# Kernel tuning notes

Hardware: AMD Instinct MI355X
Metric: run time of the kernel (lower is better)

## Reference

```python
import jax, jax.numpy as jnp
import numpy as np

B, T, V, F = 64, 2, 512, 512  # V == F required by the original loop indexing

def setup_inputs() -> dict:
    key = jax.random.key(0)
    x = jax.random.normal(key, (B, T, V, F), dtype=jnp.float32)
    return {"x": x}

def reference(x):
    # split along time axis into two halves; only the first slice of the first half is used
    xh, _ = jnp.split(x, 2, axis=1)
    x0 = xh[:, 0]  # (B, V, F)
    # Faithful to tf.norm(x[:, 0, i, :], ord=2) with NO axis: Frobenius norm over
    # the whole (batch, feature) slice -> one scalar per vertex.
    n = jnp.sqrt(jnp.sum(x0 * x0, axis=(0, 2)))  # (V,)
    # S[b,i,j] = sum_f x0[b,i,f] * x0[b,j,f]  (inner loop over j covers all V since V==F)
    gram = jnp.einsum('bif,bjf->bij', x0, x0)  # (B, V, V)
    return gram / (n[:, None] * n[None, :])
```

## Files before the change

kernel.cpp:

```cpp
#include <hip/hip_runtime.h>
#include <hip/hip_bf16.h>
#include <math.h>


#define BATCH 64
#define VDIM 512
#define FDIM 512
#define XBS (2 * VDIM * FDIM)
#define OBS (VDIM * VDIM)

typedef __bf16 bf16x8 __attribute__((ext_vector_type(8)));
typedef __bf16 bf16x4 __attribute__((ext_vector_type(4)));
typedef float f32x4 __attribute__((ext_vector_type(4)));

#define BM 128
#define BK 64
#define NKT (FDIM / BK)

#define INVN_OFF 33554432

#define GLL16(g, l)                                                          \
    __builtin_amdgcn_global_load_lds(                                        \
        (const __attribute__((address_space(1))) void*)(g),                  \
        (__attribute__((address_space(3))) void*)(l), 16, 0, 0)

__global__ __launch_bounds__(512) void cvt_norm_kernel(const float* __restrict__ x,
                                                       __bf16* __restrict__ xb,
                                                       float* __restrict__ inv_n) {
    const int v = blockIdx.x;
    const int tid = threadIdx.x;
    float s = 0.f;
    const float4* xf4 = (const float4*)x;
    for (int c = tid; c < 8192; c += 512) {
        int b = c >> 7;
        int f4 = c & 127;
        float4 d = xf4[(size_t)b * (XBS / 4) + (size_t)v * (FDIM / 4) + f4];
        s += d.x * d.x + d.y * d.y + d.z * d.z + d.w * d.w;
        bf16x4 p;
        p[0] = (__bf16)d.x; p[1] = (__bf16)d.y; p[2] = (__bf16)d.z; p[3] = (__bf16)d.w;
        *(bf16x4*)&xb[(size_t)b * (VDIM * FDIM) + (size_t)v * FDIM + f4 * 4] = p;
    }
    #pragma unroll
    for (int off = 32; off > 0; off >>= 1) s += __shfl_down(s, off, 64);
    __shared__ float partial[8];
    if ((tid & 63) == 0) partial[tid >> 6] = s;
    __syncthreads();
    if (tid == 0) {
        float t = 0.f;
        #pragma unroll
        for (int w = 0; w < 8; ++w) t += partial[w];
        inv_n[v] = 1.0f / sqrtf(t);
    }
}

__global__ __launch_bounds__(256) void gram_kernel(const __bf16* __restrict__ xb,
                                                   const float* __restrict__ inv_n,
                                                   float* __restrict__ out) {
    __shared__ __bf16 As[2][BM * BK];
    __shared__ __bf16 Bs[2][BM * BK];

    const int bid = blockIdx.x;
    const int wg = (bid & 7) * 128 + (bid >> 3);
    const int batch = wg >> 4;
    const int tile = wg & 15;
    const int ti = tile >> 2;
    const int tj = tile & 3;

    const __bf16* xbb = xb + (size_t)batch * (VDIM * FDIM);
    const int tid = threadIdx.x;
    const int lane = tid & 63;
    const int wave = tid >> 6;
    const int wr = wave >> 1;
    const int wc = wave & 1;

    const __bf16* gA[4];
    const __bf16* gB[4];
    int ldsoff[4];
    #pragma unroll
    for (int it = 0; it < 4; ++it) {
        int c = it * 256 + tid;
        int row = c >> 3;
        int cs = (c & 7) ^ (row & 7);
        gA[it] = xbb + (size_t)(ti * BM + row) * FDIM + cs * 8;
        gB[it] = xbb + (size_t)(tj * BM + row) * FDIM + cs * 8;
        ldsoff[it] = c * 8;
    }

    int offA[2][4], offB[2][4];
    #pragma unroll
    for (int ks = 0; ks < 2; ++ks) {
        #pragma unroll
        for (int m = 0; m < 4; ++m) {
            int rA = wr * 64 + m * 16 + (lane & 15);
            int rB = wc * 64 + m * 16 + (lane & 15);
            int gch = ks * 4 + (lane >> 4);
            offA[ks][m] = rA * (BK * 2) + ((gch ^ (rA & 7)) * 16);
            offB[ks][m] = rB * (BK * 2) + ((gch ^ (rB & 7)) * 16);
        }
    }

    f32x4 acc[4][4];
    #pragma unroll
    for (int m = 0; m < 4; ++m)
        #pragma unroll
        for (int n = 0; n < 4; ++n)
            acc[m][n] = (f32x4){0.f, 0.f, 0.f, 0.f};

    #pragma unroll
    for (int it = 0; it < 4; ++it) {
        GLL16(gA[it], &As[0][ldsoff[it]]);
        GLL16(gB[it], &Bs[0][ldsoff[it]]);
    }

    #pragma unroll
    for (int t = 0; t < NKT; ++t) {
        if (t < NKT - 1) {
            const int nb = (t + 1) & 1;
            #pragma unroll
            for (int it = 0; it < 4; ++it) {
                GLL16(gA[it] + (t + 1) * BK, &As[nb][ldsoff[it]]);
                GLL16(gB[it] + (t + 1) * BK, &Bs[nb][ldsoff[it]]);
            }
            asm volatile("s_waitcnt vmcnt(8)" ::: "memory");
        } else {
            asm volatile("s_waitcnt vmcnt(0)" ::: "memory");
        }
        __builtin_amdgcn_s_barrier();

        const char* Ab = (const char*)&As[t & 1][0];
        const char* Bb = (const char*)&Bs[t & 1][0];
        #pragma unroll
        for (int ks = 0; ks < 2; ++ks) {
            bf16x8 af[4], bfr[4];
            #pragma unroll
            for (int m = 0; m < 4; ++m) {
                af[m]  = *(const bf16x8*)(Ab + offA[ks][m]);
                bfr[m] = *(const bf16x8*)(Bb + offB[ks][m]);
            }
            #pragma unroll
            for (int m = 0; m < 4; ++m)
                #pragma unroll
                for (int n = 0; n < 4; ++n)
                    acc[m][n] = __builtin_amdgcn_mfma_f32_16x16x32_bf16(af[m], bfr[n], acc[m][n], 0, 0, 0);
        }
        asm volatile("s_waitcnt lgkmcnt(0)" ::: "memory");
        __builtin_amdgcn_s_barrier();
    }

    const int rowbase = ti * BM + wr * 64;
    const int colbase = tj * BM + wc * 64;
    float* ob = out + (size_t)batch * OBS;

    float si[16];
    #pragma unroll
    for (int m = 0; m < 4; ++m)
        #pragma unroll
        for (int q = 0; q < 4; ++q)
            si[m * 4 + q] = inv_n[rowbase + m * 16 + (lane >> 4) * 4 + q];

    #pragma unroll
    for (int n = 0; n < 4; ++n) {
        int j = colbase + n * 16 + (lane & 15);
        float sj = inv_n[j];
        #pragma unroll
        for (int m = 0; m < 4; ++m) {
            #pragma unroll
            for (int q = 0; q < 4; ++q) {
                int i = rowbase + m * 16 + (lane >> 4) * 4 + q;
                ob[(size_t)i * VDIM + j] = acc[m][n][q] * si[m * 4 + q] * sj;
            }
        }
    }
}

extern "C" void kernel_launch(void* const* d_in, const int* in_sizes, int n_in,
                              void* d_out, int out_size, void* d_ws, size_t ws_size,
                              hipStream_t stream) {
    const float* x = (const float*)d_in[0];
    float* out = (float*)d_out;
    __bf16* xbf = (__bf16*)d_ws;
    float* inv_n = (float*)((char*)d_ws + INVN_OFF);

    cvt_norm_kernel<<<VDIM, 512, 0, stream>>>(x, xbf, inv_n);
    gram_kernel<<<BATCH * 16, 256, 0, stream>>>(xbf, inv_n, out);
}
```

Before: 55.27 us.

## Use 256x256 tiles with 8-wave ping-pong pipelined MFMA schedule

```diff
diff --git a/kernel.cpp b/kernel.cpp
--- a/kernel.cpp
+++ b/kernel.cpp
@@ -12,10 +12,6 @@
 typedef __bf16 bf16x8 __attribute__((ext_vector_type(8)));
 typedef __bf16 bf16x4 __attribute__((ext_vector_type(4)));
 typedef float f32x4 __attribute__((ext_vector_type(4)));
-
-#define BM 128
-#define BK 64
-#define NKT (FDIM / BK)
 
 #define INVN_OFF 33554432
 
@@ -53,107 +49,151 @@
     }
 }
 
-__global__ __launch_bounds__(256) void gram_kernel(const __bf16* __restrict__ xb,
-                                                   const float* __restrict__ inv_n,
-                                                   float* __restrict__ out) {
-    __shared__ __bf16 As[2][BM * BK];
-    __shared__ __bf16 Bs[2][BM * BK];
+__global__ __launch_bounds__(512, 2) void gram_kernel(const __bf16* __restrict__ xb,
+                                                      const float* __restrict__ inv_n,
+                                                      float* __restrict__ out) {
+    __shared__ __bf16 As[2][16384];
+    __shared__ __bf16 Bs[2][16384];
 
     const int bid = blockIdx.x;
-    const int wg = (bid & 7) * 128 + (bid >> 3);
-    const int batch = wg >> 4;
-    const int tile = wg & 15;
-    const int ti = tile >> 2;
-    const int tj = tile & 3;
+    const int wg = (bid & 7) * 32 + (bid >> 3);
+    const int batch = wg >> 2;
+    const int tile = wg & 3;
+    const int tr = tile >> 1;
+    const int tc = tile & 1;
 
     const __bf16* xbb = xb + (size_t)batch * (VDIM * FDIM);
     const int tid = threadIdx.x;
     const int lane = tid & 63;
     const int wave = tid >> 6;
-    const int wr = wave >> 1;
-    const int wc = wave & 1;
-
-    const __bf16* gA[4];
-    const __bf16* gB[4];
-    int ldsoff[4];
-    #pragma unroll
-    for (int it = 0; it < 4; ++it) {
-        int c = it * 256 + tid;
-        int row = c >> 3;
-        int cs = (c & 7) ^ (row & 7);
-        gA[it] = xbb + (size_t)(ti * BM + row) * FDIM + cs * 8;
-        gB[it] = xbb + (size_t)(tj * BM + row) * FDIM + cs * 8;
-        ldsoff[it] = c * 8;
-    }
-
-    int offA[2][4], offB[2][4];
-    #pragma unroll
-    for (int ks = 0; ks < 2; ++ks) {
-        #pragma unroll
-        for (int m = 0; m < 4; ++m) {
-            int rA = wr * 64 + m * 16 + (lane & 15);
-            int rB = wc * 64 + m * 16 + (lane & 15);
-            int gch = ks * 4 + (lane >> 4);
-            offA[ks][m] = rA * (BK * 2) + ((gch ^ (rA & 7)) * 16);
-            offB[ks][m] = rB * (BK * 2) + ((gch ^ (rB & 7)) * 16);
+    const int wr = wave >> 2;
+    const int wc = wave & 3;
+
+    const int r0 = tid >> 3;
+    const int cs = (tid & 7) ^ (r0 & 7);
+    const __bf16* pA[2][2];
+    const __bf16* pB[2][2];
+    #pragma unroll
+    for (int h = 0; h < 2; ++h)
+        #pragma unroll
+        for (int j = 0; j < 2; ++j) {
+            pA[h][j] = xbb + (size_t)(tr * 256 + h * 128 + j * 64 + r0) * FDIM + cs * 8;
+            pB[h][j] = xbb + (size_t)(tc * 256 + h * 128 + j * 64 + r0) * FDIM + cs * 8;
         }
-    }
-
-    f32x4 acc[4][4];
-    #pragma unroll
-    for (int m = 0; m < 4; ++m)
+
+#define STAGE_A(KT, H) do {                                                      \
+        GLL16(pA[H][0] + (KT) * 64, &As[(KT) & 1][((H) * 1024 + tid) * 8]);      \
+        GLL16(pA[H][1] + (KT) * 64, &As[(KT) & 1][((H) * 1024 + 512 + tid) * 8]);\
+    } while (0)
+#define STAGE_B(KT, H) do {                                                      \
+        GLL16(pB[H][0] + (KT) * 64, &Bs[(KT) & 1][((H) * 1024 + tid) * 8]);      \
+        GLL16(pB[H][1] + (KT) * 64, &Bs[(KT) & 1][((H) * 1024 + 512 + tid) * 8]);\
+    } while (0)
+
+    const int gs0 = (lane >> 4) ^ (lane & 7);
+    const int abase = (wr * 128 + (lane & 15)) * 128 + gs0 * 16;
+    const int bbase = (wc * 64 + (lane & 15)) * 128 + gs0 * 16;
+
+    f32x4 acc[8][4];
+    #pragma unroll
+    for (int m = 0; m < 8; ++m)
         #pragma unroll
         for (int n = 0; n < 4; ++n)
             acc[m][n] = (f32x4){0.f, 0.f, 0.f, 0.f};
 
-    #pragma unroll
-    for (int it = 0; it < 4; ++it) {
-        GLL16(gA[it], &As[0][ldsoff[it]]);
-        GLL16(gB[it], &Bs[0][ldsoff[it]]);
-    }
-
-    #pragma unroll
-    for (int t = 0; t < NKT; ++t) {
-        if (t < NKT - 1) {
-            const int nb = (t + 1) & 1;
-            #pragma unroll
-            for (int it = 0; it < 4; ++it) {
-                GLL16(gA[it] + (t + 1) * BK, &As[nb][ldsoff[it]]);
-                GLL16(gB[it] + (t + 1) * BK, &Bs[nb][ldsoff[it]]);
-            }
-            asm volatile("s_waitcnt vmcnt(8)" ::: "memory");
-        } else {
+    STAGE_A(0, 0); STAGE_A(0, 1); STAGE_B(0, 0); STAGE_B(0, 1);
+    STAGE_B(1, 0); STAGE_B(1, 1); STAGE_A(1, 0);
+    asm volatile("s_waitcnt vmcnt(6)" ::: "memory");
+    asm volatile("s_barrier" ::: "memory");
+
+    #pragma unroll
+    for (int kt = 0; kt < 8; ++kt) {
+        const char* Ab = (const char*)&As[kt & 1][0];
+        const char* Bb = (const char*)&Bs[kt & 1][0];
+        bf16x8 af[2][4], bfl[2][2], bgh[2][2];
+
+        #pragma unroll
+        for (int ks = 0; ks < 2; ++ks) {
+            #pragma unroll
+            for (int m = 0; m < 4; ++m)
+                af[ks][m] = *(const bf16x8*)(Ab + ((abase + m * 2048) ^ (ks * 64)));
+            #pragma unroll
+            for (int n = 0; n < 2; ++n)
+                bfl[ks][n] = *(const bf16x8*)(Bb + ((bbase + n * 2048) ^ (ks * 64)));
+        }
+        if (kt + 1 < 8) STAGE_A(kt + 1, 1);
+        asm volatile("s_barrier" ::: "memory");
+        __builtin_amdgcn_s_setprio(1);
+        #pragma unroll
+        for (int ks = 0; ks < 2; ++ks)
+            #pragma unroll
+            for (int m = 0; m < 4; ++m)
+                #pragma unroll
+                for (int n = 0; n < 2; ++n)
+                    acc[m][n] = __builtin_amdgcn_mfma_f32_16x16x32_bf16(af[ks][m], bfl[ks][n], acc[m][n], 0, 0, 0);
+        __builtin_amdgcn_s_setprio(0);
+        asm volatile("s_barrier" ::: "memory");
+
+        #pragma unroll
+        for (int ks = 0; ks < 2; ++ks)
+            #pragma unroll
+            for (int n = 0; n < 2; ++n)
+                bgh[ks][n] = *(const bf16x8*)(Bb + ((bbase + (2 + n) * 2048) ^ (ks * 64)));
+        asm volatile("s_barrier" ::: "memory");
+        __builtin_amdgcn_s_setprio(1);
+        #pragma unroll
+        for (int ks = 0; ks < 2; ++ks)
+            #pragma unroll
+            for (int m = 0; m < 4; ++m)
+                #pragma unroll
+                for (int n = 0; n < 2; ++n)
+                    acc[m][2 + n] = __builtin_amdgcn_mfma_f32_16x16x32_bf16(af[ks][m], bgh[ks][n], acc[m][2 + n], 0, 0, 0);
+        __builtin_amdgcn_s_setprio(0);
+        asm volatile("s_barrier" ::: "memory");
+
+        #pragma unroll
+        for (int ks = 0; ks < 2; ++ks)
+            #pragma unroll
+            for (int m = 0; m < 4; ++m)
+                af[ks][m] = *(const bf16x8*)(Ab + ((abase + 8192 + m * 2048) ^ (ks * 64)));
+        if (kt + 2 < 8) STAGE_B(kt + 2, 0);
+        asm volatile("s_barrier" ::: "memory");
+        __builtin_amdgcn_s_setprio(1);
+        #pragma unroll
+        for (int ks = 0; ks < 2; ++ks)
+            #pragma unroll
+            for (int m = 0; m < 4; ++m)
+                #pragma unroll
+                for (int n = 0; n < 2; ++n)
+                    acc[4 + m][2 + n] = __builtin_amdgcn_mfma_f32_16x16x32_bf16(af[ks][m], bgh[ks][n], acc[4 + m][2 + n], 0, 0, 0);
+        __builtin_amdgcn_s_setprio(0);
+        asm volatile("s_barrier" ::: "memory");
+
+        if (kt + 2 < 8) { STAGE_B(kt + 2, 1); STAGE_A(kt + 2, 0); }
+        if (kt <= 5)
+            asm volatile("s_waitcnt vmcnt(6)" ::: "memory");
+        else
             asm volatile("s_waitcnt vmcnt(0)" ::: "memory");
-        }
-        __builtin_amdgcn_s_barrier();
-
-        const char* Ab = (const char*)&As[t & 1][0];
-        const char* Bb = (const char*)&Bs[t & 1][0];
-        #pragma unroll
-        for (int ks = 0; ks < 2; ++ks) {
-            bf16x8 af[4], bfr[4];
-            #pragma unroll
-            for (int m = 0; m < 4; ++m) {
-                af[m]  = *(const bf16x8*)(Ab + offA[ks][m]);
-                bfr[m] = *(const bf16x8*)(Bb + offB[ks][m]);
-            }
-            #pragma unroll
-            for (int m = 0; m < 4; ++m)
-                #pragma unroll
-                for (int n = 0; n < 4; ++n)
-                    acc[m][n] = __builtin_amdgcn_mfma_f32_16x16x32_bf16(af[m], bfr[n], acc[m][n], 0, 0, 0);
-        }
-        asm volatile("s_waitcnt lgkmcnt(0)" ::: "memory");
-        __builtin_amdgcn_s_barrier();
-    }
-
-    const int rowbase = ti * BM + wr * 64;
-    const int colbase = tj * BM + wc * 64;
+        asm volatile("s_barrier" ::: "memory");
+        __builtin_amdgcn_s_setprio(1);
+        #pragma unroll
+        for (int ks = 0; ks < 2; ++ks)
+            #pragma unroll
+            for (int m = 0; m < 4; ++m)
+                #pragma unroll
+                for (int n = 0; n < 2; ++n)
+                    acc[4 + m][n] = __builtin_amdgcn_mfma_f32_16x16x32_bf16(af[ks][m], bfl[ks][n], acc[4 + m][n], 0, 0, 0);
+        __builtin_amdgcn_s_setprio(0);
+        asm volatile("s_barrier" ::: "memory");
+    }
+
+    const int rowbase = tr * 256 + wr * 128;
+    const int colbase = tc * 256 + wc * 64;
     float* ob = out + (size_t)batch * OBS;
 
-    float si[16];
-    #pragma unroll
-    for (int m = 0; m < 4; ++m)
+    float si[32];
+    #pragma unroll
+    for (int m = 0; m < 8; ++m)
         #pragma unroll
         for (int q = 0; q < 4; ++q)
             si[m * 4 + q] = inv_n[rowbase + m * 16 + (lane >> 4) * 4 + q];
@@ -163,7 +203,7 @@
         int j = colbase + n * 16 + (lane & 15);
         float sj = inv_n[j];
         #pragma unroll
-        for (int m = 0; m < 4; ++m) {
+        for (int m = 0; m < 8; ++m) {
             #pragma unroll
             for (int q = 0; q < 4; ++q) {
                 int i = rowbase + m * 16 + (lane >> 4) * 4 + q;
@@ -171,6 +211,8 @@
             }
         }
     }
+#undef STAGE_A
+#undef STAGE_B
 }
 
 extern "C" void kernel_launch(void* const* d_in, const int* in_sizes, int n_in,
@@ -182,5 +224,5 @@
     float* inv_n = (float*)((char*)d_ws + INVN_OFF);
 
     cvt_norm_kernel<<<VDIM, 512, 0, stream>>>(x, xbf, inv_n);
-    gram_kernel<<<BATCH * 16, 256, 0, stream>>>(xbf, inv_n, out);
+    gram_kernel<<<BATCH * 4, 512, 0, stream>>>(xbf, inv_n, out);
 }
```

Result: faster. 52.38 us (-5.2%).
